# Kernel optimization log

Measured on AMD Instinct MI355X. Metric: run time of the kernel, lower is better.

## Reference

```python
import jax, jax.numpy as jnp
import numpy as np

B, C, H, W = 4, 256, 64, 64
CI = C // 2  # inter_channels


def setup_inputs() -> dict:
    key = jax.random.key(0)
    ks = jax.random.split(key, 10)
    s_in = 1.0 / np.sqrt(C)
    s_out = 1.0 / np.sqrt(CI)
    return {
        "rgbd": jax.random.normal(ks[0], (B, C, H, W), jnp.float32),
        "x": jax.random.normal(ks[1], (B, C, H, W), jnp.float32),
        "q_w": jax.random.uniform(ks[2], (CI, C), jnp.float32, -s_in, s_in),
        "q_b": jax.random.uniform(ks[3], (CI,), jnp.float32, -s_in, s_in),
        "k_w": jax.random.uniform(ks[4], (CI, C), jnp.float32, -s_in, s_in),
        "k_b": jax.random.uniform(ks[5], (CI,), jnp.float32, -s_in, s_in),
        "v_w": jax.random.uniform(ks[6], (CI, C), jnp.float32, -s_in, s_in),
        "v_b": jax.random.uniform(ks[7], (CI,), jnp.float32, -s_in, s_in),
        "out_w": jax.random.uniform(ks[8], (C, CI), jnp.float32, -s_out, s_out),
        "out_b": jax.random.uniform(ks[9], (C,), jnp.float32, -s_out, s_out),
    }


def reference(rgbd, x, q_w, q_b, k_w, k_b, v_w, v_b, out_w, out_b):
    b, c, h, w = rgbd.shape
    ci = q_w.shape[0]
    n = h * w
    # 1x1 convs == channel-wise linear maps; flatten spatial to tokens
    xs = x.reshape(b, c, n)        # [B, C, N]
    rs = rgbd.reshape(b, c, n)     # [B, C, N]
    q = jnp.einsum('oc,bcn->bno', q_w, xs) + q_b          # [B, N, CI]
    k = jnp.einsum('oc,bcn->bon', k_w, rs) + k_b[:, None]  # [B, CI, N]
    v = jnp.einsum('oc,bcn->bno', v_w, rs) + v_b          # [B, N, CI]
    attn = jax.nn.softmax(jnp.einsum('bqc,bck->bqk', q, k), axis=-1)  # [B, N, N]
    out = jnp.einsum('bqk,bkc->bqc', attn, v)             # [B, N, CI]
    out = jnp.einsum('oc,bnc->bon', out_w, out) + out_b[:, None]  # [B, C, N]
    return rgbd + out.reshape(b, c, h, w)
```

## Files before the change

kernel.cpp:

```cpp
#include <hip/hip_runtime.h>
#include <cstdint>
#include <cstddef>

typedef unsigned short u16;
typedef __attribute__((ext_vector_type(8))) short bf16x8;
typedef __attribute__((ext_vector_type(4))) float f32x4;
typedef __attribute__((ext_vector_type(16))) float f32x16;
typedef __attribute__((ext_vector_type(4))) uint32_t u32x4;

#define DEV __device__ __forceinline__

static constexpr float LOG2E = 1.4426950408889634f;

DEV u16 f2bf(float f) {
  uint32_t u = __float_as_uint(f);
  u += 0x7fffu + ((u >> 16) & 1u);
  return (u16)(u >> 16);
}
DEV float bf2f(u16 h) {
  uint32_t u = ((uint32_t)h) << 16;
  return __uint_as_float(u);
}
DEV uint32_t cvtpk(float lo, float hi) {
  uint32_t r;
  asm("v_cvt_pk_bf16_f32 %0, %1, %2" : "=v"(r) : "v"(lo), "v"(hi));
  return r;
}
DEV float exp2fast(float x) {
  float r;
  asm("v_exp_f32 %0, %1" : "=v"(r) : "v"(x));
  return r;
}
DEV void plswap(uint32_t& a, uint32_t& b) {
  asm("v_permlane32_swap_b32 %0, %1" : "+v"(a), "+v"(b));
}

DEV f32x4 mfma16(bf16x8 a, bf16x8 b, f32x4 c) {
  return __builtin_amdgcn_mfma_f32_16x16x32_bf16(a, b, c, 0, 0, 0);
}
DEV f32x16 mfma32(bf16x8 a, bf16x8 b, f32x16 c) {
  return __builtin_amdgcn_mfma_f32_32x32x16_bf16(a, b, c, 0, 0, 0);
}

DEV void gload_lds16(const void* g, void* l) {
  __builtin_amdgcn_global_load_lds(
      (const __attribute__((address_space(1))) uint32_t*)g,
      (__attribute__((address_space(3))) uint32_t*)l, 16, 0, 0);
}

static constexpr int BATCH = 4;
static constexpr int C = 256;
static constexpr int CI = 128;
static constexpr int N = 4096;
static constexpr int SPLIT = 4;
static constexpr int KPB = N / SPLIT;
static constexpr int NT = KPB / 32;

__global__ __launch_bounds__(256) void cvt_w(const float* __restrict__ a,
                                             const float* __restrict__ b,
                                             const float* __restrict__ c,
                                             const float* __restrict__ d,
                                             u16* __restrict__ oa, u16* __restrict__ ob,
                                             u16* __restrict__ oc, u16* __restrict__ od) {
  int i = blockIdx.x * 256 + threadIdx.x;
  oa[i] = f2bf(a[i] * LOG2E);
  ob[i] = f2bf(b[i]);
  oc[i] = f2bf(c[i]);
  od[i] = f2bf(d[i]);
}

__global__ __launch_bounds__(256) void proj_kernel(
    const float* __restrict__ x, const float* __restrict__ rgbd,
    const u16* __restrict__ Wq, const u16* __restrict__ Wk, const u16* __restrict__ Wv,
    const float* __restrict__ qb, const float* __restrict__ kb, const float* __restrict__ vb,
    u16* __restrict__ Qb, u16* __restrict__ Kb, u16* __restrict__ Vtb) {
  __shared__ __align__(16) u16 xT[64][C + 8];
  __shared__ __align__(16) u16 rT[64][C + 8];
  const int b = blockIdx.y;
  const int n0 = blockIdx.x * 64;
  const int t = threadIdx.x;
  {
    const int tok = t & 63, cp = (t >> 6) * 2;
    const float* xb = x + (size_t)b * C * N + n0;
    const float* rb = rgbd + (size_t)b * C * N + n0;
    for (int c0 = 0; c0 < C; c0 += 8) {
      int c = c0 + cp;
      *(uint32_t*)&xT[tok][c] = cvtpk(xb[(size_t)c * N + tok], xb[(size_t)(c + 1) * N + tok]);
      *(uint32_t*)&rT[tok][c] = cvtpk(rb[(size_t)c * N + tok], rb[(size_t)(c + 1) * N + tok]);
    }
  }
  __syncthreads();
  const int w = t >> 6, lane = t & 63, g = lane >> 4, cl = lane & 15;

#define PROJ_QK(Sarr, W, bias, Out, SCL)                                              \
  {                                                                                   \
    bf16x8 afr[8];                                                                    \
    _Pragma("unroll") for (int ks = 0; ks < 8; ++ks)                                  \
        afr[ks] = *(const bf16x8*)&Sarr[w * 16 + cl][ks * 32 + g * 8];                \
    _Pragma("unroll") for (int ct = 0; ct < 8; ++ct) {                                \
      f32x4 acc = {0.f, 0.f, 0.f, 0.f};                                               \
      _Pragma("unroll") for (int ks = 0; ks < 8; ++ks) {                              \
        bf16x8 bb = *(const bf16x8*)&W[(size_t)(ct * 16 + cl) * C + ks * 32 + g * 8]; \
        acc = mfma16(afr[ks], bb, acc);                                               \
      }                                                                               \
      float bv = bias[ct * 16 + cl] * (SCL);                                          \
      _Pragma("unroll") for (int r = 0; r < 4; ++r) {                                 \
        int tok = n0 + w * 16 + g * 4 + r;                                            \
        Out[((size_t)b * N + tok) * CI + ct * 16 + cl] = f2bf(acc[r] + bv);           \
      }                                                                               \
    }                                                                                 \
  }

  PROJ_QK(xT, Wq, qb, Qb, LOG2E)
  PROJ_QK(rT, Wk, kb, Kb, 1.0f)
#undef PROJ_QK

  #pragma unroll
  for (int rt = 0; rt < 2; ++rt) {
    bf16x8 aw[8];
    #pragma unroll
    for (int ks = 0; ks < 8; ++ks)
      aw[ks] = *(const bf16x8*)&Wv[(size_t)(w * 32 + rt * 16 + cl) * C + ks * 32 + g * 8];
    #pragma unroll
    for (int ct = 0; ct < 4; ++ct) {
      f32x4 acc = {0.f, 0.f, 0.f, 0.f};
      #pragma unroll
      for (int ks = 0; ks < 8; ++ks) {
        bf16x8 bb = *(const bf16x8*)&rT[ct * 16 + cl][ks * 32 + g * 8];
        acc = mfma16(aw[ks], bb, acc);
      }
      #pragma unroll
      for (int r = 0; r < 4; ++r) {
        int o = w * 32 + rt * 16 + g * 4 + r;
        Vtb[((size_t)b * CI + o) * N + n0 + ct * 16 + cl] = f2bf(acc[r] + vb[o]);
      }
    }
  }
}

__global__ __launch_bounds__(256, 2) void attn_kernel(
    const u16* __restrict__ Qb, const u16* __restrict__ Kb,
    const u16* __restrict__ Vtb, u16* __restrict__ Opart,
    float2* __restrict__ ml) {
  __shared__ __align__(16) u16 Klds[2][32 * 128];
  __shared__ __align__(16) u16 Vlds[2][128 * 32];
  const int lin = blockIdx.x;
  const int nl = (lin & 7) * 64 + (lin >> 3);
  const int qi = nl & 31;
  const int grp = nl >> 5;
  const int b = grp & 3;
  const int s = grp >> 2;
  const int q0 = qi * 128;
  const int t = threadIdx.x;
  const int w = t >> 6, lane = t & 63;
  const int hi = lane >> 5, l31 = lane & 31;

  const u16* Kg = Kb + (size_t)b * N * CI;
  const u16* Vg = Vtb + (size_t)b * CI * N;

  const int k_r = t >> 4;
  const int k_ss = (t & 15) ^ k_r;
  const int v_r = t >> 2;
  const int v_ss = (t & 3) ^ ((t >> 3) & 3);
  const int wbase = (t & ~63);

#define STAGE_K(bi, k0_)                                                          \
  do {                                                                            \
    _Pragma("unroll") for (int c = 0; c < 2; ++c) {                               \
      gload_lds16(Kg + (size_t)((k0_) + c * 16 + k_r) * CI + k_ss * 8,            \
                  &Klds[bi][(c * 256 + wbase) * 8]);                              \
    }                                                                             \
  } while (0)
#define STAGE_V(bi, k0_)                                                          \
  do {                                                                            \
    _Pragma("unroll") for (int c = 0; c < 2; ++c) {                               \
      gload_lds16(Vg + (size_t)(c * 64 + v_r) * N + (k0_) + v_ss * 8,             \
                  &Vlds[bi][(c * 256 + wbase) * 8]);                              \
    }                                                                             \
  } while (0)

  const u16* Qg = Qb + ((size_t)b * N + q0 + w * 32 + l31) * CI;
  bf16x8 qf[8];
  #pragma unroll
  for (int mm = 0; mm < 8; ++mm)
    qf[mm] = *(const bf16x8*)(Qg + mm * 16 + hi * 8);
  asm volatile("s_waitcnt vmcnt(0)" ::: "memory");

  f32x16 oacc[4];
  #pragma unroll
  for (int ct = 0; ct < 4; ++ct)
    #pragma unroll
    for (int i = 0; i < 16; ++i) oacc[ct][i] = 0.f;
  float m_run = -1e30f, l_run = 0.f;

  const int kbeg = s * KPB;
  STAGE_K(0, kbeg);
  STAGE_V(0, kbeg);
  STAGE_K(1, kbeg + 32);
  STAGE_V(1, kbeg + 32);

  int buf = 0;
  for (int tt = 0; tt < NT; ++tt) {
    asm volatile("s_waitcnt vmcnt(4)" ::: "memory");
    __builtin_amdgcn_s_barrier();
    const int knext = kbeg + ((tt + 2 < NT) ? tt + 2 : tt) * 32;

    bf16x8 kf[8];
    #pragma unroll
    for (int mm = 0; mm < 8; ++mm)
      kf[mm] = *(const bf16x8*)&Klds[buf][l31 * 128 + ((((mm << 1) | hi) ^ l31) & 15) * 8];
    asm volatile("s_waitcnt lgkmcnt(0)" ::: "memory");
    __builtin_amdgcn_s_barrier();
    STAGE_K(buf, knext);

    f32x16 st;
    #pragma unroll
    for (int i = 0; i < 16; ++i) st[i] = 0.f;
    __builtin_amdgcn_s_setprio(1);
    #pragma unroll
    for (int mm = 0; mm < 8; ++mm) st = mfma32(kf[mm], qf[mm], st);
    __builtin_amdgcn_s_setprio(0);

    float tmax = st[0];
    #pragma unroll
    for (int i = 1; i < 16; ++i) tmax = fmaxf(tmax, st[i]);
    tmax = fmaxf(tmax, __shfl_xor(tmax, 32));
    if (!__all(tmax - m_run <= 11.5f)) {
      const float mn = fmaxf(m_run, tmax);
      const float alpha = exp2fast(m_run - mn);
      m_run = mn;
      l_run *= alpha;
      #pragma unroll
      for (int reg = 0; reg < 16; ++reg) {
        float ar = __shfl(alpha, (reg & 3) + 8 * (reg >> 2) + 4 * hi);
        oacc[0][reg] *= ar; oacc[1][reg] *= ar;
        oacc[2][reg] *= ar; oacc[3][reg] *= ar;
      }
    }
    float p[16];
    float ls = 0.f;
    #pragma unroll
    for (int i = 0; i < 16; ++i) {
      p[i] = exp2fast(st[i] - m_run);
      ls += p[i];
    }
    ls += __shfl_xor(ls, 32);
    l_run += ls;

    uint32_t d0 = cvtpk(p[0], p[1]),  e0 = cvtpk(p[4], p[5]);
    uint32_t d1 = cvtpk(p[2], p[3]),  e1 = cvtpk(p[6], p[7]);
    uint32_t d2 = cvtpk(p[8], p[9]),  e2 = cvtpk(p[12], p[13]);
    uint32_t d3 = cvtpk(p[10], p[11]), e3 = cvtpk(p[14], p[15]);
    plswap(d0, e0);
    plswap(d1, e1);
    plswap(d2, e2);
    plswap(d3, e3);
    u32x4 pw0 = {d0, d1, e0, e1};
    u32x4 pw1 = {d2, d3, e2, e3};
    bf16x8 pa0 = __builtin_bit_cast(bf16x8, pw0);
    bf16x8 pa1 = __builtin_bit_cast(bf16x8, pw1);

    bf16x8 vf[4][2];
    const int vsw = (l31 >> 1) & 3;
    #pragma unroll
    for (int ct = 0; ct < 4; ++ct)
      #pragma unroll
      for (int ks = 0; ks < 2; ++ks)
        vf[ct][ks] = *(const bf16x8*)
            &Vlds[buf][(32 * ct + l31) * 32 + ((((ks << 1) | hi) ^ vsw) & 3) * 8];
    asm volatile("s_waitcnt lgkmcnt(0)" ::: "memory");
    __builtin_amdgcn_s_barrier();
    STAGE_V(buf, knext);

    __builtin_amdgcn_s_setprio(1);
    #pragma unroll
    for (int ct = 0; ct < 4; ++ct) {
      oacc[ct] = mfma32(pa0, vf[ct][0], oacc[ct]);
      oacc[ct] = mfma32(pa1, vf[ct][1], oacc[ct]);
    }
    __builtin_amdgcn_s_setprio(0);

    buf ^= 1;
  }
#undef STAGE_K
#undef STAGE_V
  asm volatile("s_waitcnt vmcnt(0)" ::: "memory");

  const float inv = 1.0f / l_run;
  #pragma unroll
  for (int reg = 0; reg < 16; ++reg) {
    const int ql = (reg & 3) + 8 * (reg >> 2) + 4 * hi;
    const float invr = __shfl(inv, ql);
    const int q = q0 + w * 32 + ql;
    #pragma unroll
    for (int ct = 0; ct < 4; ++ct)
      Opart[(((size_t)(s * BATCH + b)) * N + q) * CI + 32 * ct + l31] =
          f2bf(oacc[ct][reg] * invr);
  }
  if (lane < 32) {
    const int q = q0 + w * 32 + lane;
    ml[(size_t)(s * BATCH + b) * N + q] = make_float2(m_run, l_run);
  }
}

template <int NS>
__global__ __launch_bounds__(256) void combine_kernel(
    const u16* __restrict__ Opart, const float2* __restrict__ ml,
    u16* __restrict__ Ob) {
  const int idx = blockIdx.x * 256 + threadIdx.x;
  const int ci8 = idx & 15;
  const int row = idx >> 4;
  float2 sv[NS];
  float M = -1e30f;
  #pragma unroll
  for (int sp = 0; sp < NS; ++sp) {
    sv[sp] = ml[(size_t)sp * BATCH * N + row];
    M = fmaxf(M, sv[sp].x);
  }
  float wv[NS], wsum = 0.f;
  #pragma unroll
  for (int sp = 0; sp < NS; ++sp) {
    wv[sp] = sv[sp].y * exp2fast(sv[sp].x - M);
    wsum += wv[sp];
  }
  const float invL = 1.0f / wsum;
  float acc[8];
  #pragma unroll
  for (int j = 0; j < 8; ++j) acc[j] = 0.f;
  #pragma unroll
  for (int sp = 0; sp < NS; ++sp) {
    const float ws = wv[sp] * invL;
    bf16x8 v = *(const bf16x8*)&Opart[((size_t)sp * BATCH * N + row) * CI + ci8 * 8];
    #pragma unroll
    for (int j = 0; j < 8; ++j) acc[j] += ws * bf2f((u16)v[j]);
  }
  bf16x8 o;
  #pragma unroll
  for (int j = 0; j < 8; ++j) o[j] = (short)f2bf(acc[j]);
  *(bf16x8*)&Ob[(size_t)row * CI + ci8 * 8] = o;
}

__global__ __launch_bounds__(256) void outproj_kernel(
    const u16* __restrict__ Ob, const u16* __restrict__ Wo,
    const float* __restrict__ obias, const float* __restrict__ rgbd,
    float* __restrict__ out) {
  const int b = blockIdx.y;
  const int n0 = blockIdx.x * 64;
  const int t = threadIdx.x;
  const int w = t >> 6, lane = t & 63, g = lane >> 4, cl = lane & 15;

  f32x4 acc[4][4];
  #pragma unroll
  for (int i = 0; i < 4; ++i)
    #pragma unroll
    for (int j = 0; j < 4; ++j) acc[i][j] = {0.f, 0.f, 0.f, 0.f};

  #pragma unroll
  for (int ks = 0; ks < 4; ++ks) {
    bf16x8 bo[4];
    #pragma unroll
    for (int ct = 0; ct < 4; ++ct)
      bo[ct] = *(const bf16x8*)&Ob[((size_t)b * N + n0 + ct * 16 + cl) * CI + ks * 32 + g * 8];
    #pragma unroll
    for (int rt = 0; rt < 4; ++rt) {
      bf16x8 aw = *(const bf16x8*)&Wo[(size_t)(w * 64 + rt * 16 + cl) * CI + ks * 32 + g * 8];
      #pragma unroll
      for (int ct = 0; ct < 4; ++ct) acc[rt][ct] = mfma16(aw, bo[ct], acc[rt][ct]);
    }
  }
  #pragma unroll
  for (int rt = 0; rt < 4; ++rt) {
    #pragma unroll
    for (int r = 0; r < 4; ++r) {
      const int o = w * 64 + rt * 16 + g * 4 + r;
      const float bb = obias[o];
      #pragma unroll
      for (int ct = 0; ct < 4; ++ct) {
        size_t idx = ((size_t)b * C + o) * N + n0 + ct * 16 + cl;
        out[idx] = rgbd[idx] + bb + acc[rt][ct][r];
      }
    }
  }
}

extern "C" void kernel_launch(void* const* d_in, const int* in_sizes, int n_in,
                              void* d_out, int out_size, void* d_ws, size_t ws_size,
                              hipStream_t stream) {
  (void)in_sizes; (void)n_in; (void)out_size; (void)ws_size;
  const float* rgbd = (const float*)d_in[0];
  const float* x    = (const float*)d_in[1];
  const float* q_w  = (const float*)d_in[2];
  const float* q_b  = (const float*)d_in[3];
  const float* k_w  = (const float*)d_in[4];
  const float* k_b  = (const float*)d_in[5];
  const float* v_w  = (const float*)d_in[6];
  const float* v_b  = (const float*)d_in[7];
  const float* o_w  = (const float*)d_in[8];
  const float* o_b  = (const float*)d_in[9];
  float* out = (float*)d_out;

  char* ws = (char*)d_ws;
  const size_t MB = 1024 * 1024;
  const size_t szQKV = (size_t)BATCH * N * CI * sizeof(u16);
  u16* Qb  = (u16*)(ws);
  u16* Kb  = (u16*)(ws + szQKV);
  u16* Vtb = (u16*)(ws + 2 * szQKV);
  u16* Wq  = (u16*)(ws + 3 * szQKV);
  u16* Wk  = Wq + (size_t)CI * C;
  u16* Wv  = Wk + (size_t)CI * C;
  u16* Wo  = Wv + (size_t)CI * C;
  u16* Opart = (u16*)(ws + 13 * MB);
  float2* ml = (float2*)(ws + 29 * MB);
  u16* Ob  = Qb;

  const int grid_attn = 32 * BATCH * SPLIT;

  cvt_w<<<dim3((C * CI) / 256), 256, 0, stream>>>(q_w, k_w, v_w, o_w, Wq, Wk, Wv, Wo);
  proj_kernel<<<dim3(N / 64, BATCH), 256, 0, stream>>>(x, rgbd, Wq, Wk, Wv,
                                                       q_b, k_b, v_b, Qb, Kb, Vtb);
  attn_kernel<<<dim3(grid_attn), 256, 0, stream>>>(Qb, Kb, Vtb, Opart, ml);
  combine_kernel<SPLIT><<<dim3(BATCH * N * (CI / 8) / 256), 256, 0, stream>>>(Opart, ml, Ob);
  outproj_kernel<<<dim3(N / 64, BATCH), 256, 0, stream>>>(Ob, Wo, o_b, rgbd, out);
}
```

Baseline: 94.85 us.

## Software-pipeline PV MFMAs into next QK step and fuse combine into outproj

The attention loop now defers each tile's P·V MFMAs to the next iteration, issuing them alongside the following QK^T MFMAs, with a final drain after the loop. The goal is to overlap softmax/exp work with matrix-core work. It also adds sched_barriers around the LDS waits. Separately, the split-K combine kernel is folded into the output-projection kernel, which merges partials into LDS and so drops one launch and the Ob global round-trip. The cost is extra register pressure from the carried P and V fragments, and redundant ml loads per block.

Result: faster. 89.66 us (-5.5%).

```diff
diff --git a/kernel.cpp b/kernel.cpp
--- a/kernel.cpp
+++ b/kernel.cpp
@@ -53,8 +53,6 @@
 static constexpr int CI = 128;
 static constexpr int N = 4096;
 static constexpr int SPLIT = 4;
-static constexpr int KPB = N / SPLIT;
-static constexpr int NT = KPB / 32;
 
 __global__ __launch_bounds__(256) void cvt_w(const float* __restrict__ a,
                                              const float* __restrict__ b,
@@ -138,14 +136,18 @@
   }
 }
 
+template <int SPL>
 __global__ __launch_bounds__(256, 2) void attn_kernel(
     const u16* __restrict__ Qb, const u16* __restrict__ Kb,
     const u16* __restrict__ Vtb, u16* __restrict__ Opart,
     float2* __restrict__ ml) {
+  constexpr int KPB = N / SPL;
+  constexpr int NT = KPB / 32;
+  constexpr int CPX = 16 * SPL;
   __shared__ __align__(16) u16 Klds[2][32 * 128];
   __shared__ __align__(16) u16 Vlds[2][128 * 32];
   const int lin = blockIdx.x;
-  const int nl = (lin & 7) * 64 + (lin >> 3);
+  const int nl = (lin & 7) * CPX + (lin >> 3);
   const int qi = nl & 31;
   const int grp = nl >> 5;
   const int b = grp & 3;
@@ -199,6 +201,9 @@
   STAGE_K(1, kbeg + 32);
   STAGE_V(1, kbeg + 32);
 
+  bf16x8 paA = {}, paB = {};
+  bf16x8 vfp[4][2];
+
   int buf = 0;
   for (int tt = 0; tt < NT; ++tt) {
     asm volatile("s_waitcnt vmcnt(4)" ::: "memory");
@@ -210,6 +215,7 @@
     for (int mm = 0; mm < 8; ++mm)
       kf[mm] = *(const bf16x8*)&Klds[buf][l31 * 128 + ((((mm << 1) | hi) ^ l31) & 15) * 8];
     asm volatile("s_waitcnt lgkmcnt(0)" ::: "memory");
+    __builtin_amdgcn_sched_barrier(0);
     __builtin_amdgcn_s_barrier();
     STAGE_K(buf, knext);
 
@@ -217,6 +223,13 @@
     #pragma unroll
     for (int i = 0; i < 16; ++i) st[i] = 0.f;
     __builtin_amdgcn_s_setprio(1);
+    if (tt > 0) {
+      #pragma unroll
+      for (int ct = 0; ct < 4; ++ct) {
+        oacc[ct] = mfma32(paA, vfp[ct][0], oacc[ct]);
+        oacc[ct] = mfma32(paB, vfp[ct][1], oacc[ct]);
+      }
+    }
     #pragma unroll
     for (int mm = 0; mm < 8; ++mm) st = mfma32(kf[mm], qf[mm], st);
     __builtin_amdgcn_s_setprio(0);
@@ -247,43 +260,45 @@
     ls += __shfl_xor(ls, 32);
     l_run += ls;
 
-    uint32_t d0 = cvtpk(p[0], p[1]),  e0 = cvtpk(p[4], p[5]);
-    uint32_t d1 = cvtpk(p[2], p[3]),  e1 = cvtpk(p[6], p[7]);
-    uint32_t d2 = cvtpk(p[8], p[9]),  e2 = cvtpk(p[12], p[13]);
-    uint32_t d3 = cvtpk(p[10], p[11]), e3 = cvtpk(p[14], p[15]);
-    plswap(d0, e0);
-    plswap(d1, e1);
-    plswap(d2, e2);
-    plswap(d3, e3);
-    u32x4 pw0 = {d0, d1, e0, e1};
-    u32x4 pw1 = {d2, d3, e2, e3};
-    bf16x8 pa0 = __builtin_bit_cast(bf16x8, pw0);
-    bf16x8 pa1 = __builtin_bit_cast(bf16x8, pw1);
-
-    bf16x8 vf[4][2];
+    {
+      uint32_t d0 = cvtpk(p[0], p[1]),   e0 = cvtpk(p[4], p[5]);
+      uint32_t d1 = cvtpk(p[2], p[3]),   e1 = cvtpk(p[6], p[7]);
+      uint32_t d2 = cvtpk(p[8], p[9]),   e2 = cvtpk(p[12], p[13]);
+      uint32_t d3 = cvtpk(p[10], p[11]), e3 = cvtpk(p[14], p[15]);
+      plswap(d0, e0);
+      plswap(d1, e1);
+      plswap(d2, e2);
+      plswap(d3, e3);
+      u32x4 pw0 = {d0, d1, e0, e1};
+      u32x4 pw1 = {d2, d3, e2, e3};
+      paA = __builtin_bit_cast(bf16x8, pw0);
+      paB = __builtin_bit_cast(bf16x8, pw1);
+    }
+
     const int vsw = (l31 >> 1) & 3;
     #pragma unroll
     for (int ct = 0; ct < 4; ++ct)
       #pragma unroll
       for (int ks = 0; ks < 2; ++ks)
-        vf[ct][ks] = *(const bf16x8*)
+        vfp[ct][ks] = *(const bf16x8*)
             &Vlds[buf][(32 * ct + l31) * 32 + ((((ks << 1) | hi) ^ vsw) & 3) * 8];
     asm volatile("s_waitcnt lgkmcnt(0)" ::: "memory");
+    __builtin_amdgcn_sched_barrier(0);
     __builtin_amdgcn_s_barrier();
     STAGE_V(buf, knext);
 
-    __builtin_amdgcn_s_setprio(1);
-    #pragma unroll
-    for (int ct = 0; ct < 4; ++ct) {
-      oacc[ct] = mfma32(pa0, vf[ct][0], oacc[ct]);
-      oacc[ct] = mfma32(pa1, vf[ct][1], oacc[ct]);
-    }
-    __builtin_amdgcn_s_setprio(0);
-
     buf ^= 1;
   }
 #undef STAGE_K
 #undef STAGE_V
+
+  __builtin_amdgcn_s_setprio(1);
+  #pragma unroll
+  for (int ct = 0; ct < 4; ++ct) {
+    oacc[ct] = mfma32(paA, vfp[ct][0], oacc[ct]);
+    oacc[ct] = mfma32(paB, vfp[ct][1], oacc[ct]);
+  }
+  __builtin_amdgcn_s_setprio(0);
   asm volatile("s_waitcnt vmcnt(0)" ::: "memory");
 
   const float inv = 1.0f / l_run;
@@ -303,52 +318,52 @@
   }
 }
 
-template <int NS>
-__global__ __launch_bounds__(256) void combine_kernel(
+__global__ __launch_bounds__(256) void outproj_kernel(
     const u16* __restrict__ Opart, const float2* __restrict__ ml,
-    u16* __restrict__ Ob) {
-  const int idx = blockIdx.x * 256 + threadIdx.x;
-  const int ci8 = idx & 15;
-  const int row = idx >> 4;
-  float2 sv[NS];
-  float M = -1e30f;
-  #pragma unroll
-  for (int sp = 0; sp < NS; ++sp) {
-    sv[sp] = ml[(size_t)sp * BATCH * N + row];
-    M = fmaxf(M, sv[sp].x);
-  }
-  float wv[NS], wsum = 0.f;
-  #pragma unroll
-  for (int sp = 0; sp < NS; ++sp) {
-    wv[sp] = sv[sp].y * exp2fast(sv[sp].x - M);
-    wsum += wv[sp];
-  }
-  const float invL = 1.0f / wsum;
-  float acc[8];
-  #pragma unroll
-  for (int j = 0; j < 8; ++j) acc[j] = 0.f;
-  #pragma unroll
-  for (int sp = 0; sp < NS; ++sp) {
-    const float ws = wv[sp] * invL;
-    bf16x8 v = *(const bf16x8*)&Opart[((size_t)sp * BATCH * N + row) * CI + ci8 * 8];
-    #pragma unroll
-    for (int j = 0; j < 8; ++j) acc[j] += ws * bf2f((u16)v[j]);
-  }
-  bf16x8 o;
-  #pragma unroll
-  for (int j = 0; j < 8; ++j) o[j] = (short)f2bf(acc[j]);
-  *(bf16x8*)&Ob[(size_t)row * CI + ci8 * 8] = o;
-}
-
-__global__ __launch_bounds__(256) void outproj_kernel(
-    const u16* __restrict__ Ob, const u16* __restrict__ Wo,
-    const float* __restrict__ obias, const float* __restrict__ rgbd,
-    float* __restrict__ out) {
+    const u16* __restrict__ Wo, const float* __restrict__ obias,
+    const float* __restrict__ rgbd, float* __restrict__ out) {
+  __shared__ __align__(16) u16 ObL[64][CI + 8];
   const int b = blockIdx.y;
   const int n0 = blockIdx.x * 64;
   const int t = threadIdx.x;
+
+  #pragma unroll
+  for (int i = 0; i < 4; ++i) {
+    const int idx = t + i * 256;
+    const int row_l = idx >> 4, ci8 = idx & 15;
+    const size_t row = (size_t)b * N + n0 + row_l;
+    float2 sv[SPLIT];
+    float M = -1e30f;
+    #pragma unroll
+    for (int sp = 0; sp < SPLIT; ++sp) {
+      sv[sp] = ml[(size_t)sp * BATCH * N + row];
+      M = fmaxf(M, sv[sp].x);
+    }
+    float wv[SPLIT], wsum = 0.f;
+    #pragma unroll
+    for (int sp = 0; sp < SPLIT; ++sp) {
+      wv[sp] = sv[sp].y * exp2fast(sv[sp].x - M);
+      wsum += wv[sp];
+    }
+    const float invL = 1.0f / wsum;
+    float acc[8];
+    #pragma unroll
+    for (int j = 0; j < 8; ++j) acc[j] = 0.f;
+    #pragma unroll
+    for (int sp = 0; sp < SPLIT; ++sp) {
+      const float wsc = wv[sp] * invL;
+      bf16x8 v = *(const bf16x8*)&Opart[((size_t)sp * BATCH * N + row) * CI + ci8 * 8];
+      #pragma unroll
+      for (int j = 0; j < 8; ++j) acc[j] += wsc * bf2f((u16)v[j]);
+    }
+    bf16x8 o;
+    #pragma unroll
+    for (int j = 0; j < 8; ++j) o[j] = (short)f2bf(acc[j]);
+    *(bf16x8*)&ObL[row_l][ci8 * 8] = o;
+  }
+  __syncthreads();
+
   const int w = t >> 6, lane = t & 63, g = lane >> 4, cl = lane & 15;
-
   f32x4 acc[4][4];
   #pragma unroll
   for (int i = 0; i < 4; ++i)
@@ -360,7 +375,7 @@
     bf16x8 bo[4];
     #pragma unroll
     for (int ct = 0; ct < 4; ++ct)
-      bo[ct] = *(const bf16x8*)&Ob[((size_t)b * N + n0 + ct * 16 + cl) * CI + ks * 32 + g * 8];
+      bo[ct] = *(const bf16x8*)&ObL[ct * 16 + cl][ks * 32 + g * 8];
     #pragma unroll
     for (int rt = 0; rt < 4; ++rt) {
       bf16x8 aw = *(const bf16x8*)&Wo[(size_t)(w * 64 + rt * 16 + cl) * CI + ks * 32 + g * 8];
@@ -411,14 +426,10 @@
   u16* Wo  = Wv + (size_t)CI * C;
   u16* Opart = (u16*)(ws + 13 * MB);
   float2* ml = (float2*)(ws + 29 * MB);
-  u16* Ob  = Qb;
-
-  const int grid_attn = 32 * BATCH * SPLIT;
 
   cvt_w<<<dim3((C * CI) / 256), 256, 0, stream>>>(q_w, k_w, v_w, o_w, Wq, Wk, Wv, Wo);
   proj_kernel<<<dim3(N / 64, BATCH), 256, 0, stream>>>(x, rgbd, Wq, Wk, Wv,
                                                        q_b, k_b, v_b, Qb, Kb, Vtb);
-  attn_kernel<<<dim3(grid_attn), 256, 0, stream>>>(Qb, Kb, Vtb, Opart, ml);
-  combine_kernel<SPLIT><<<dim3(BATCH * N * (CI / 8) / 256), 256, 0, stream>>>(Opart, ml, Ob);
-  outproj_kernel<<<dim3(N / 64, BATCH), 256, 0, stream>>>(Ob, Wo, o_b, rgbd, out);
-}
+  attn_kernel<SPLIT><<<dim3(128 * SPLIT), 256, 0, stream>>>(Qb, Kb, Vtb, Opart, ml);
+  outproj_kernel<<<dim3(N / 64, BATCH), 256, 0, stream>>>(Opart, ml, Wo, o_b, rgbd, out);
+}
```
